# Performance work log

Hardware: AMD Instinct MI355X
Metric: run time of the kernel (lower is better)

The kernel has to match this reference:

```python
import jax, jax.numpy as jnp
import numpy as np

EMBED_DIM = 2048
NUM_HEADS = 16
HEAD_DIM = EMBED_DIM // NUM_HEADS  # 128
GROUP = 256
NEG = -1e9


def setup_inputs() -> dict:
    key = jax.random.key(0)
    ks = jax.random.split(key, 4)
    B, N, C = 2, 8192, EMBED_DIM
    s = 1.0 / np.sqrt(C).astype(np.float32)
    return {
        "x": jax.random.normal(ks[0], (B, N, C), jnp.float32),
        "Wq": jax.random.normal(ks[1], (C, C), jnp.float32) * s,
        "bq": jnp.zeros((C,), jnp.float32),
        "Wk": jax.random.normal(ks[2], (C, C), jnp.float32) * s,
        "bk": jnp.zeros((C,), jnp.float32),
        "Wv": jax.random.normal(ks[3], (C, C), jnp.float32) * s,
        "bv": jnp.zeros((C,), jnp.float32),
    }


def _s2_attn(x, Wq, bq, Wk, bk, Wv, bv):
    B, N, C = x.shape
    H, hd, gs = NUM_HEADS, HEAD_DIM, GROUP
    G = N // gs
    half = H // 2

    def heads(t):  # [B,N,C] -> [B,H,N,hd]
        return t.reshape(B, N, H, hd).transpose(0, 2, 1, 3)

    q = heads(x @ Wq.T + bq)
    k = heads(x @ Wk.T + bk)
    v = heads(x @ Wv.T + bv)

    def shift(t, s):  # shift second half of heads along sequence
        return jnp.concatenate([t[:, :half], jnp.roll(t[:, half:], s, axis=2)], axis=1)

    q, k, v = shift(q, -(gs // 2)), shift(k, -(gs // 2)), shift(v, -(gs // 2))

    # group-local attention: [B,H,G,gs,hd]
    qg = q.reshape(B, H, G, gs, hd)
    kg = k.reshape(B, H, G, gs, hd)
    vg = v.reshape(B, H, G, gs, hd)

    scores = jnp.einsum("bhgqd,bhgkd->bhgqk", qg, kg) / np.sqrt(hd).astype(x.dtype)
    causal = jnp.triu(jnp.ones((gs, gs), bool), 1)  # mask strictly-upper triangle
    scores = jnp.where(causal, NEG, scores)
    attn = jax.nn.softmax(scores, axis=-1)
    out = jnp.einsum("bhgqk,bhgkd->bhgqd", attn, vg).reshape(B, H, N, hd)

    out = shift(out, gs // 2)  # un-shift the shifted heads
    return out.transpose(0, 2, 1, 3).reshape(B, N, C)


def reference(x, Wq, bq, Wk, bk, Wv, bv):
    return _s2_attn(x, Wq, bq, Wk, bk, Wv, bv)
```

## Files before the change

kernel.cpp:

```cpp
#include <hip/hip_runtime.h>
#include <hip/hip_bf16.h>

#define NSEQ 8192
#define CDIM 2048
#define NHEAD 16
#define HD 128

typedef short short8 __attribute__((ext_vector_type(8)));
typedef short short4v __attribute__((ext_vector_type(4)));
typedef float float4v __attribute__((ext_vector_type(4)));

__device__ __forceinline__ short f2bf(float f) {
    __hip_bfloat16 h = __float2bfloat16(f);
    return *reinterpret_cast<short*>(&h);
}

__device__ __forceinline__ void async_load16(const short* g, short* l) {
    __builtin_amdgcn_global_load_lds((const __attribute__((address_space(1))) void*)g,
                                     (__attribute__((address_space(3))) void*)l,
                                     16, 0, 0);
}

#define X8 (33554432 / 8)
#define W8 (4194304 / 8)

__global__ __launch_bounds__(256) void cvt_all(
    const float* __restrict__ x, const float* __restrict__ wq,
    const float* __restrict__ wk, const float* __restrict__ wv,
    short* __restrict__ xb, short* __restrict__ wqb,
    short* __restrict__ wkb, short* __restrict__ wvb)
{
    const size_t i = (size_t)blockIdx.x * blockDim.x + threadIdx.x;
    const float* src;
    short* dst;
    size_t off;
    if (i < X8)              { src = x;  dst = xb;  off = i; }
    else if (i < X8 + W8)    { src = wq; dst = wqb; off = i - X8; }
    else if (i < X8 + 2*W8)  { src = wk; dst = wkb; off = i - X8 - W8; }
    else                     { src = wv; dst = wvb; off = i - X8 - 2*(size_t)W8; }
    const float4v a = ((const float4v*)src)[off * 2];
    const float4v b = ((const float4v*)src)[off * 2 + 1];
    short8 o;
    for (int j = 0; j < 4; j++) { o[j] = f2bf(a[j]); o[4 + j] = f2bf(b[j]); }
    ((short8*)dst)[off] = o;
}

#define PBAR()  asm volatile("s_barrier" ::: "memory")
#define LGKM0() do { asm volatile("s_waitcnt lgkmcnt(0)" ::: "memory"); \
                     __builtin_amdgcn_sched_barrier(0); } while (0)
#define VMC4()  asm volatile("s_waitcnt vmcnt(4)" ::: "memory")

#define MFMA(d, x, y) d = __builtin_amdgcn_mfma_f32_16x16x32_bf16(x, y, d, 0, 0, 0)

__global__ __launch_bounds__(512, 2) void qkv_gemm8(
    const short* __restrict__ xb,
    const short* __restrict__ Wq, const float* __restrict__ bq,
    const short* __restrict__ Wk, const float* __restrict__ bk,
    const short* __restrict__ Wv, const float* __restrict__ bv,
    float* __restrict__ qout, short* __restrict__ kt, short* __restrict__ vt)
{
    __shared__ short lds[2][2][256 * 64];

    const int tid  = threadIdx.x;
    const int w    = tid >> 6;
    const int lane = tid & 63;
    const int quad = lane >> 4;
    const int l15  = lane & 15;
    const int wm   = w >> 2;
    const int wn   = w & 3;

    const int id    = (blockIdx.x & 7) * 192 + (blockIdx.x >> 3);
    const int mtile = id / 24;
    const int rest  = id - mtile * 24;
    const int mat   = rest >> 3;
    const int ntile = rest & 7;
    const int M0 = mtile << 8;
    const int N0 = ntile << 8;

    const short* W    = (mat == 0) ? Wq : (mat == 1) ? Wk : Wv;
    const float* bias = (mat == 0) ? bq : (mat == 1) ? bk : bv;
    const short* Ab = xb + (size_t)M0 * CDIM;
    const short* Bb = W  + (size_t)N0 * CDIM;

    const int stg_row = tid >> 3;
    const int stg_col = ((tid & 7) * 8) ^ (((tid >> 3) & 1) << 5) ^ (((tid >> 6) & 1) << 4);
    const int cswz    = ((lane & 1) << 5) | (((lane >> 3) & 1) << 4);

    float bvals[4];
#pragma unroll
    for (int j = 0; j < 4; ++j)
        bvals[j] = bias[N0 + wn * 64 + j * 16 + l15];
    asm volatile("s_waitcnt vmcnt(0)" ::: "memory");

    float4v acc[8][4];
#pragma unroll
    for (int i = 0; i < 8; ++i)
#pragma unroll
        for (int j = 0; j < 4; ++j)
            acc[i][j] = (float4v){0.f, 0.f, 0.f, 0.f};

    auto stage = [&](int bufi, int ab, int h, int t, const short* src) {
        short* l0 = &lds[bufi][ab][h * 8192 + w * 512];
        const short* g = src + (size_t)(h * 128 + stg_row) * CDIM + t * 64 + stg_col;
        async_load16(g, l0);
        async_load16(g + (size_t)64 * CDIM, l0 + 4096);
    };
    auto ldA = [&](int bufi, int i, int ks) -> short8 {
        const int row = wm * 128 + i * 16 + l15;
        return *(const short8*)&lds[bufi][0][row * 64 + ((ks * 32 + quad * 8) ^ cswz)];
    };
    auto ldB = [&](int bufi, int j, int ks) -> short8 {
        const int row = wn * 64 + j * 16 + l15;
        return *(const short8*)&lds[bufi][1][row * 64 + ((ks * 32 + quad * 8) ^ cswz)];
    };

    stage(0, 0, 0, 0, Ab); stage(0, 0, 1, 0, Ab);
    stage(0, 1, 0, 0, Bb); stage(0, 1, 1, 0, Bb);
    stage(1, 1, 0, 1, Bb); stage(1, 1, 1, 1, Bb);
    VMC4();
    PBAR();

    short8 a[4][2], b[4][2];
    for (int it = 0; it < 16; ++it) {
        const int t1 = 2 * it + 1;
        const int t2 = (2 * it + 2 > 31) ? 31 : 2 * it + 2;
        const int t3 = (2 * it + 3 > 31) ? 31 : 2 * it + 3;

#pragma unroll
        for (int i = 0; i < 4; ++i) { a[i][0] = ldA(0, i, 0); a[i][1] = ldA(0, i, 1); }
#pragma unroll
        for (int j = 0; j < 2; ++j) { b[j][0] = ldB(0, j, 0); b[j][1] = ldB(0, j, 1); }
        stage(1, 0, 0, t1, Ab); stage(1, 0, 1, t1, Ab);
        PBAR(); LGKM0();
        __builtin_amdgcn_s_setprio(1);
#pragma unroll
        for (int i = 0; i < 4; ++i)
#pragma unroll
            for (int j = 0; j < 2; ++j) { MFMA(acc[i][j], a[i][0], b[j][0]);
                                          MFMA(acc[i][j], a[i][1], b[j][1]); }
        __builtin_amdgcn_s_setprio(0);
        PBAR();

#pragma unroll
        for (int j = 2; j < 4; ++j) { b[j][0] = ldB(0, j, 0); b[j][1] = ldB(0, j, 1); }
        PBAR(); LGKM0();
        __builtin_amdgcn_s_setprio(1);
#pragma unroll
        for (int i = 0; i < 4; ++i)
#pragma unroll
            for (int j = 2; j < 4; ++j) { MFMA(acc[i][j], a[i][0], b[j][0]);
                                          MFMA(acc[i][j], a[i][1], b[j][1]); }
        __builtin_amdgcn_s_setprio(0);
        PBAR();

#pragma unroll
        for (int i = 0; i < 4; ++i) { a[i][0] = ldA(0, 4 + i, 0); a[i][1] = ldA(0, 4 + i, 1); }
        stage(0, 1, 0, t2, Bb);
        PBAR(); LGKM0();
        __builtin_amdgcn_s_setprio(1);
#pragma unroll
        for (int i = 0; i < 4; ++i)
#pragma unroll
            for (int j = 2; j < 4; ++j) { MFMA(acc[4 + i][j], a[i][0], b[j][0]);
                                          MFMA(acc[4 + i][j], a[i][1], b[j][1]); }
        __builtin_amdgcn_s_setprio(0);
        PBAR();

        stage(0, 1, 1, t2, Bb);
        PBAR(); LGKM0();
        __builtin_amdgcn_s_setprio(1);
#pragma unroll
        for (int i = 0; i < 4; ++i)
#pragma unroll
            for (int j = 0; j < 2; ++j) { MFMA(acc[4 + i][j], a[i][0], b[j][0]);
                                          MFMA(acc[4 + i][j], a[i][1], b[j][1]); }
        __builtin_amdgcn_s_setprio(0);
        VMC4();
        PBAR();

#pragma unroll
        for (int i = 0; i < 4; ++i) { a[i][0] = ldA(1, i, 0); a[i][1] = ldA(1, i, 1); }
#pragma unroll
        for (int j = 0; j < 2; ++j) { b[j][0] = ldB(1, j, 0); b[j][1] = ldB(1, j, 1); }
        stage(0, 0, 0, t2, Ab); stage(0, 0, 1, t2, Ab);
        PBAR(); LGKM0();
        __builtin_amdgcn_s_setprio(1);
#pragma unroll
        for (int i = 0; i < 4; ++i)
#pragma unroll
            for (int j = 0; j < 2; ++j) { MFMA(acc[i][j], a[i][0], b[j][0]);
                                          MFMA(acc[i][j], a[i][1], b[j][1]); }
        __builtin_amdgcn_s_setprio(0);
        PBAR();

#pragma unroll
        for (int j = 2; j < 4; ++j) { b[j][0] = ldB(1, j, 0); b[j][1] = ldB(1, j, 1); }
        PBAR(); LGKM0();
        __builtin_amdgcn_s_setprio(1);
#pragma unroll
        for (int i = 0; i < 4; ++i)
#pragma unroll
            for (int j = 2; j < 4; ++j) { MFMA(acc[i][j], a[i][0], b[j][0]);
                                          MFMA(acc[i][j], a[i][1], b[j][1]); }
        __builtin_amdgcn_s_setprio(0);
        PBAR();

#pragma unroll
        for (int i = 0; i < 4; ++i) { a[i][0] = ldA(1, 4 + i, 0); a[i][1] = ldA(1, 4 + i, 1); }
        stage(1, 1, 0, t3, Bb);
        PBAR(); LGKM0();
        __builtin_amdgcn_s_setprio(1);
#pragma unroll
        for (int i = 0; i < 4; ++i)
#pragma unroll
            for (int j = 2; j < 4; ++j) { MFMA(acc[4 + i][j], a[i][0], b[j][0]);
                                          MFMA(acc[4 + i][j], a[i][1], b[j][1]); }
        __builtin_amdgcn_s_setprio(0);
        PBAR();

        stage(1, 1, 1, t3, Bb);
        PBAR(); LGKM0();
        __builtin_amdgcn_s_setprio(1);
#pragma unroll
        for (int i = 0; i < 4; ++i)
#pragma unroll
            for (int j = 0; j < 2; ++j) { MFMA(acc[4 + i][j], a[i][0], b[j][0]);
                                          MFMA(acc[4 + i][j], a[i][1], b[j][1]); }
        __builtin_amdgcn_s_setprio(0);
        VMC4();
        PBAR();
    }

#pragma unroll
    for (int j = 0; j < 4; ++j) {
        const int n = N0 + wn * 64 + j * 16 + l15;
        if (mat == 0) {
#pragma unroll
            for (int i = 0; i < 8; ++i) {
                const int mrow = M0 + wm * 128 + i * 16 + quad * 4;
#pragma unroll
                for (int r = 0; r < 4; ++r)
                    qout[((size_t)(mrow + r) << 11) + n] = acc[i][j][r] + bvals[j];
            }
        } else {
            short* outp = (mat == 1) ? kt : vt;
            const int h = n >> 7;
            const int d = n & (HD - 1);
#pragma unroll
            for (int i = 0; i < 8; ++i) {
                const int mrow = M0 + wm * 128 + i * 16 + quad * 4;
#pragma unroll
                for (int r = 0; r < 4; ++r) {
                    const int m  = mrow + r;
                    const int bb = m >> 13;
                    const int sq = m & (NSEQ - 1);
                    outp[(((size_t)(bb * NHEAD + h) * NSEQ + sq) << 7) + d] =
                        f2bf(acc[i][j][r] + bvals[j]);
                }
            }
        }
    }
}

__global__ __launch_bounds__(512, 2) void s2_attn(const float* qsrc,
                                                  const short* __restrict__ kt,
                                                  const short* __restrict__ vt,
                                                  float* out)
{
    __shared__ short Ks[64 * 136];
    __shared__ short Vs[64 * 132];
    __shared__ short Ps[8][32 * 40];

    const int bx = blockIdx.x;
    const int g  = bx & 31;
    const int h  = (bx >> 5) & 15;
    const int b  = bx >> 9;
    const int shift = (h >= 8) ? 128 : 0;
    const int sbase = g * 256 + shift;

    const int tid  = threadIdx.x;
    const int wave = tid >> 6;
    const int lane = tid & 63;
    const int quad = lane >> 4;
    const int l15  = lane & 15;

    const size_t bh = ((size_t)b * NHEAD + h) * NSEQ;
    const short* kg = kt + bh * HD;
    const short* vg = vt + bh * HD;

    const int mt0 = wave * 2;

    short8 qf[2][4];
    for (int im = 0; im < 2; im++) {
        const int row = (mt0 + im) * 16 + l15;
        const int p   = (sbase + row) & (NSEQ - 1);
        const float* qr = qsrc + (((size_t)(b * NSEQ + p)) << 11) + h * HD;
        for (int ks = 0; ks < 4; ks++) {
            const float4v qa = *(const float4v*)(qr + ks * 32 + quad * 8);
            const float4v qb = *(const float4v*)(qr + ks * 32 + quad * 8 + 4);
            short8 f;
            for (int j = 0; j < 4; j++) { f[j] = f2bf(qa[j]); f[4 + j] = f2bf(qb[j]); }
            qf[im][ks] = f;
        }
    }

    const float4v fzero = {0.f, 0.f, 0.f, 0.f};
    float4v o[2][8];
    for (int im = 0; im < 2; im++)
        for (int dt = 0; dt < 8; dt++)
            o[im][dt] = fzero;
    float rs[2][4] = {{0.f, 0.f, 0.f, 0.f}, {0.f, 0.f, 0.f, 0.f}};

    for (int kc = 0; kc < 4; kc++) {
        __syncthreads();
        for (int c = 0; c < 2; c++) {
            const int id   = tid + c * 512;
            const int row  = id >> 4;
            const int colb = (id & 15) * 8;
            const int p    = (sbase + kc * 64 + row) & (NSEQ - 1);
            *(short8*)&Ks[row * 136 + colb] = *(const short8*)(kg + (size_t)p * HD + colb);
        }
        for (int c = 0; c < 4; c++) {
            const int id   = tid + c * 512;
            const int row  = id >> 5;
            const int colb = (id & 31) * 4;
            const int p    = (sbase + kc * 64 + row) & (NSEQ - 1);
            *(short4v*)&Vs[row * 132 + colb] = *(const short4v*)(vg + (size_t)p * HD + colb);
        }
        __syncthreads();

        float4v s[2][4];
        for (int im = 0; im < 2; im++)
            for (int nn = 0; nn < 4; nn++)
                s[im][nn] = fzero;
        for (int nn = 0; nn < 4; nn++) {
            short8 kf[4];
            for (int ks = 0; ks < 4; ks++)
                kf[ks] = *(const short8*)&Ks[(nn * 16 + l15) * 136 + ks * 32 + quad * 8];
            for (int im = 0; im < 2; im++)
                for (int ks = 0; ks < 4; ks++)
                    s[im][nn] = __builtin_amdgcn_mfma_f32_16x16x32_bf16(
                        qf[im][ks], kf[ks], s[im][nn], 0, 0, 0);
        }

        for (int half = 0; half < 2; half++) {
            for (int im = 0; im < 2; im++) {
                const int qpos = (mt0 + im) * 16 + quad * 4;
                for (int nn2 = 0; nn2 < 2; nn2++) {
                    const int nn   = half * 2 + nn2;
                    const int kpos = kc * 64 + nn * 16 + l15;
                    for (int r = 0; r < 4; r++) {
                        const float sv = s[im][nn][r] * 0.088388347648318447f;
                        const float pv = (kpos > qpos + r)
                                             ? 0.f
                                             : __expf(fminf(sv, 30.f));
                        rs[im][r] += pv;
                        Ps[wave][(im * 16 + quad * 4 + r) * 40 + nn2 * 16 + l15] = f2bf(pv);
                    }
                }
            }
            __syncthreads();
            short8 pf[2];
            for (int im = 0; im < 2; im++)
                pf[im] = *(const short8*)&Ps[wave][(im * 16 + l15) * 40 + quad * 8];
            for (int dt = 0; dt < 8; dt++) {
                short8 vf;
                for (int jj = 0; jj < 8; jj++)
                    vf[jj] = Vs[(half * 32 + quad * 8 + jj) * 132 + dt * 16 + l15];
                for (int im = 0; im < 2; im++)
                    o[im][dt] = __builtin_amdgcn_mfma_f32_16x16x32_bf16(
                        pf[im], vf, o[im][dt], 0, 0, 0);
            }
            __syncthreads();
        }
    }

    for (int im = 0; im < 2; im++)
        for (int r = 0; r < 4; r++) {
            float v = rs[im][r];
            v += __shfl_xor(v, 1);
            v += __shfl_xor(v, 2);
            v += __shfl_xor(v, 4);
            v += __shfl_xor(v, 8);
            rs[im][r] = v;
        }

    for (int im = 0; im < 2; im++) {
        for (int r = 0; r < 4; r++) {
            const int row = (mt0 + im) * 16 + quad * 4 + r;
            const int p   = (sbase + row) & (NSEQ - 1);
            const float inv = 1.f / rs[im][r];
            const size_t obase = (((size_t)(b * NSEQ + p)) << 11) + h * HD;
            for (int dt = 0; dt < 8; dt++)
                out[obase + dt * 16 + l15] = o[im][dt][r] * inv;
        }
    }
}

extern "C" void kernel_launch(void* const* d_in, const int* in_sizes, int n_in,
                              void* d_out, int out_size, void* d_ws, size_t ws_size,
                              hipStream_t stream) {
    (void)in_sizes; (void)n_in; (void)out_size; (void)ws_size;
    const float* x  = (const float*)d_in[0];
    const float* Wq = (const float*)d_in[1];
    const float* bq = (const float*)d_in[2];
    const float* Wk = (const float*)d_in[3];
    const float* bk = (const float*)d_in[4];
    const float* Wv = (const float*)d_in[5];
    const float* bv = (const float*)d_in[6];

    short* xb  = (short*)d_ws;
    short* wqb = xb  + (size_t)33554432;
    short* wkb = wqb + (size_t)4194304;
    short* wvb = wkb + (size_t)4194304;
    short* kt  = wvb + (size_t)4194304;
    short* vt  = kt  + (size_t)33554432;

    float* outp = (float*)d_out;

    cvt_all<<<dim3(22528), 256, 0, stream>>>(x, Wq, Wk, Wv, xb, wqb, wkb, wvb);
    qkv_gemm8<<<dim3(1536), 512, 0, stream>>>(xb, wqb, bq, wkb, bk, wvb, bv,
                                              outp, kt, vt);
    s2_attn<<<dim3(1024), 512, 0, stream>>>(outp, kt, vt, outp);
}
```

Baseline: 774.2 us.

## Store V transposed and load V fragments as swizzled vector LDS reads

Result: no change. 767.2 us (-0.9%).

```diff
diff --git a/kernel.cpp b/kernel.cpp
--- a/kernel.cpp
+++ b/kernel.cpp
@@ -83,8 +83,8 @@
     const short* Bb = W  + (size_t)N0 * CDIM;
 
     const int stg_row = tid >> 3;
-    const int stg_col = ((tid & 7) * 8) ^ (((tid >> 3) & 1) << 5) ^ (((tid >> 6) & 1) << 4);
-    const int cswz    = ((lane & 1) << 5) | (((lane >> 3) & 1) << 4);
+    const int stg_col = ((tid & 7) * 8) ^ (((tid >> 3) & 7) << 3);
+    const int cswz    = (lane & 7) << 3;
 
     float bvals[4];
 #pragma unroll
@@ -242,8 +242,7 @@
                 for (int r = 0; r < 4; ++r)
                     qout[((size_t)(mrow + r) << 11) + n] = acc[i][j][r] + bvals[j];
             }
-        } else {
-            short* outp = (mat == 1) ? kt : vt;
+        } else if (mat == 1) {
             const int h = n >> 7;
             const int d = n & (HD - 1);
 #pragma unroll
@@ -254,9 +253,22 @@
                     const int m  = mrow + r;
                     const int bb = m >> 13;
                     const int sq = m & (NSEQ - 1);
-                    outp[(((size_t)(bb * NHEAD + h) * NSEQ + sq) << 7) + d] =
+                    kt[(((size_t)(bb * NHEAD + h) * NSEQ + sq) << 7) + d] =
                         f2bf(acc[i][j][r] + bvals[j]);
                 }
+            }
+        } else {
+            const int h = n >> 7;
+            const int d = n & (HD - 1);
+#pragma unroll
+            for (int i = 0; i < 8; ++i) {
+                const int mrow = M0 + wm * 128 + i * 16 + quad * 4;
+                const int bb = mrow >> 13;
+                const int sq = mrow & (NSEQ - 1);
+                short4v o4;
+#pragma unroll
+                for (int r = 0; r < 4; ++r) o4[r] = f2bf(acc[i][j][r] + bvals[j]);
+                *(short4v*)&vt[(((size_t)(bb * NHEAD + h) * HD + d) << 13) + sq] = o4;
             }
         }
     }
@@ -268,7 +280,7 @@
                                                   float* out)
 {
     __shared__ short Ks[64 * 136];
-    __shared__ short Vs[64 * 132];
+    __shared__ short Vt[128 * 64];
     __shared__ short Ps[8][32 * 40];
 
     const int bx = blockIdx.x;
@@ -311,6 +323,9 @@
             o[im][dt] = fzero;
     float rs[2][4] = {{0.f, 0.f, 0.f, 0.f}, {0.f, 0.f, 0.f, 0.f}};
 
+    const int vrow_in_w = lane >> 3;
+    const int vgcol     = ((lane & 7) * 8) ^ (vrow_in_w << 3);
+
     for (int kc = 0; kc < 4; kc++) {
         __syncthreads();
         for (int c = 0; c < 2; c++) {
@@ -320,12 +335,10 @@
             const int p    = (sbase + kc * 64 + row) & (NSEQ - 1);
             *(short8*)&Ks[row * 136 + colb] = *(const short8*)(kg + (size_t)p * HD + colb);
         }
-        for (int c = 0; c < 4; c++) {
-            const int id   = tid + c * 512;
-            const int row  = id >> 5;
-            const int colb = (id & 31) * 4;
-            const int p    = (sbase + kc * 64 + row) & (NSEQ - 1);
-            *(short4v*)&Vs[row * 132 + colb] = *(const short4v*)(vg + (size_t)p * HD + colb);
+        for (int c = 0; c < 2; c++) {
+            const int d = c * 64 + wave * 8 + vrow_in_w;
+            const int p = (sbase + kc * 64 + vgcol) & (NSEQ - 1);
+            async_load16(vg + (size_t)d * NSEQ + p, &Vt[(c * 64 + wave * 8) * 64]);
         }
         __syncthreads();
 
@@ -364,9 +377,9 @@
             for (int im = 0; im < 2; im++)
                 pf[im] = *(const short8*)&Ps[wave][(im * 16 + l15) * 40 + quad * 8];
             for (int dt = 0; dt < 8; dt++) {
-                short8 vf;
-                for (int jj = 0; jj < 8; jj++)
-                    vf[jj] = Vs[(half * 32 + quad * 8 + jj) * 132 + dt * 16 + l15];
+                const int d = dt * 16 + l15;
+                const short8 vf = *(const short8*)
+                    &Vt[d * 64 + ((half * 32 + quad * 8) ^ ((l15 & 7) << 3))];
                 for (int im = 0; im < 2; im++)
                     o[im][dt] = __builtin_amdgcn_mfma_f32_16x16x32_bf16(
                         pf[im], vf, o[im][dt], 0, 0, 0);
```
